# Performance work log

Measured on AMD Instinct MI355X. Metric: run time of the kernel, lower is better.

## Reference

```python
import math
import jax, jax.numpy as jnp
import numpy as np

BATCH, L, H, M, K = 16, 4096, 256, 256, 4

def setup_inputs() -> dict:
    key = jax.random.key(0)
    ks = jax.random.split(key, 12)
    inputs = jax.random.normal(ks[0], (BATCH, L, H), jnp.float32)
    b_std = 1.0 / math.sqrt(H)
    c_std = 1.0 / math.sqrt(M)
    B_param = jax.random.uniform(ks[1], (M, H, 2), jnp.float32, -b_std, b_std)
    C_param = jax.random.uniform(ks[2], (H, M, 2), jnp.float32, -c_std, c_std)
    D = jax.random.normal(ks[3], (H,), jnp.float32)
    enc_w = jax.random.normal(ks[4], (H, H), jnp.float32) * (1.0 / math.sqrt(H))
    enc_b = jnp.zeros((H,), jnp.float32)
    conv_w = jax.random.normal(ks[5], (H, 1, K), jnp.float32) * (1.0 / math.sqrt(K))
    conv_b = jnp.zeros((H,), jnp.float32)
    # ring init: r in [0.9,1.0], theta in (0,pi)
    r0 = jnp.sqrt(jax.random.uniform(ks[6], (M,), jnp.float32) * (1.0 - 0.81) + 0.81)
    r0 = jnp.clip(r0, 0.9, 0.999)
    th0 = jax.random.uniform(ks[7], (M,), jnp.float32, 0.05, math.pi - 0.05)
    r_logit_base = jnp.log(r0 / (1.0 - r0))
    th_atanh_base = jnp.arctanh(th0 / math.pi)
    # heads are zero-init in the module; use small random so the selective path is exercised
    r_head_w = jax.random.normal(ks[8], (M, H), jnp.float32) * 0.01
    th_head_w = jax.random.normal(ks[9], (M, H), jnp.float32) * 0.01
    dt_base = jax.random.normal(ks[10], (M,), jnp.float32) * 0.5
    inj_head_w = jax.random.normal(ks[11], (M, H), jnp.float32) * 0.01
    return {"inputs": inputs, "B_param": B_param, "C_param": C_param, "D": D,
            "enc_w": enc_w, "enc_b": enc_b, "conv_w": conv_w, "conv_b": conv_b,
            "r_logit_base": r_logit_base, "th_atanh_base": th_atanh_base,
            "r_head_w": r_head_w, "th_head_w": th_head_w, "dt_base": dt_base,
            "inj_head_w": inj_head_w}

def _forward(inputs, B_param, C_param, D, enc_w, enc_b, conv_w, conv_b,
             r_logit_base, th_atanh_base, r_head_w, th_head_w, dt_base, inj_head_w):
    silu = jax.nn.silu
    # encoder: linear -> SiLU -> depthwise causal conv (left pad K-1) -> SiLU
    feats = silu(inputs @ enc_w.T + enc_b)                      # (B,L,H)
    fc = jnp.transpose(feats, (0, 2, 1))                        # (B,H,L)
    conv = jax.lax.conv_general_dilated(
        fc, conv_w, window_strides=(1,), padding=[(K - 1, 0)],
        dimension_numbers=("NCH", "OIH", "NCH"), feature_group_count=H)
    feats = silu(jnp.transpose(conv + conv_b[None, :, None], (0, 2, 1)))  # (B,L,H)
    # spectral conditioning
    r = jax.nn.sigmoid(r_logit_base + feats @ r_head_w.T)       # (B,L,M)
    theta = math.pi * jnp.tanh(th_atanh_base + feats @ th_head_w.T)
    dt = jax.nn.sigmoid(dt_base)                                # (M,) per_step_dt=False
    dtc = jnp.maximum(dt, 1e-6)
    r2 = jnp.maximum(r * r, 1e-8)
    A = jnp.maximum((r2 - 2.0 * r * jnp.cos(theta) + 1.0) / (dtc * dtc * r2), 0.0)
    G = jnp.maximum((1.0 - r2) / (dtc * r2), 0.0)
    # complex input projection + selective injection gate
    bu = jax.lax.complex(inputs @ B_param[..., 0].T, inputs @ B_param[..., 1].T)  # (B,L,M) c64
    gate = jax.nn.sigmoid(feats @ inj_head_w.T)
    bu = bu * gate
    # time-major for scan
    A_s = jnp.transpose(A, (1, 0, 2))
    G_s = jnp.transpose(G, (1, 0, 2))
    bu_s = jnp.transpose(bu, (1, 0, 2))
    z0 = jnp.zeros((inputs.shape[0], M), jnp.complex64)
    x0 = jnp.zeros((inputs.shape[0], M), jnp.complex64)

    def step(carry, t_in):  # imex1 variant
        z, x = carry
        A_t, G_t, bu_t = t_in
        S = 1.0 + dtc * G_t
        z = (z + dtc * (-A_t * x + bu_t)) / jnp.maximum(S, 1e-6)
        x = x + dtc * z
        return (z, x), x

    _, xs = jax.lax.scan(step, (z0, x0), (A_s, G_s, bu_s))      # (L,B,M) complex64
    proj = (jnp.einsum("lbm,hm->lbh", xs.real, C_param[..., 0])
            - jnp.einsum("lbm,hm->lbh", xs.imag, C_param[..., 1]))
    proj = jnp.transpose(proj, (1, 0, 2))                       # (B,L,H)
    return proj + D * inputs

def reference(inputs, B_param, C_param, D, enc_w, enc_b, conv_w, conv_b,
              r_logit_base, th_atanh_base, r_head_w, th_head_w, dt_base, inj_head_w):
    return _forward(inputs, B_param, C_param, D, enc_w, enc_b, conv_w, conv_b,
                    r_logit_base, th_atanh_base, r_head_w, th_head_w, dt_base, inj_head_w)
```

## Files before the change

### kernel.cpp

```cpp
#include <hip/hip_runtime.h>

#define H_ 256
#define M_ 256
#define L_ 4096
#define B_ 16
#define PI_F 3.14159265358979323846f

typedef unsigned short u16;
typedef __attribute__((ext_vector_type(8))) short short8v;
typedef __attribute__((ext_vector_type(4))) float floatx4;

__device__ __forceinline__ float sigm(float x) { return 1.0f / (1.0f + expf(-x)); }
__device__ __forceinline__ u16 f2bf(float f) {
    unsigned int u = __float_as_uint(f);
    unsigned int r = (u + 0x7fff + ((u >> 16) & 1)) >> 16;
    return (u16)r;
}
__device__ __forceinline__ float bf2f(u16 h) { return __uint_as_float(((unsigned int)h) << 16); }
__device__ __forceinline__ void split2(float x, u16& h, u16& l) {
    h = f2bf(x);
    l = f2bf(x - bf2f(h));
}

__global__ __launch_bounds__(256) void k_prep(const float* __restrict__ Bp,
                                              const float* __restrict__ Cp,
                                              const float* __restrict__ enc_w,
                                              const float* __restrict__ Wr,
                                              const float* __restrict__ Wt,
                                              const float* __restrict__ Wg,
                                              const float* __restrict__ dtb,
                                              u16* __restrict__ EWhi, u16* __restrict__ EWlo,
                                              u16* __restrict__ HWhi, u16* __restrict__ HWlo,
                                              u16* __restrict__ GWhi,
                                              u16* __restrict__ WBh,
                                              u16* __restrict__ Chath,
                                              float* __restrict__ dtc, float* __restrict__ idt,
                                              float* __restrict__ idt2) {
    int tid = blockIdx.x * 256 + threadIdx.x;
    if (tid < M_) {
        float d = fmaxf(sigm(dtb[tid]), 1e-6f);
        dtc[tid] = d;
        idt[tid] = 1.0f / d;
        idt2[tid] = 1.0f / (d * d);
    }
    u16 h, l;
    split2(enc_w[tid], h, l); EWhi[tid] = h; EWlo[tid] = l;
    split2(Wr[tid], h, l);    HWhi[tid] = h; HWlo[tid] = l;
    split2(Wt[tid], h, l);    HWhi[65536 + tid] = h; HWlo[65536 + tid] = l;
    GWhi[tid] = f2bf(Wg[tid]);
    WBh[tid]         = f2bf(Bp[2 * tid + 0]);
    WBh[65536 + tid] = f2bf(Bp[2 * tid + 1]);
    int hh = tid >> 8, m = tid & (M_ - 1);
    Chath[hh * 512 + 2 * m + 0] = f2bf(Cp[2 * tid + 0]);
    Chath[hh * 512 + 2 * m + 1] = f2bf(-Cp[2 * tid + 1]);
}

__global__ __launch_bounds__(256) void k_zero(float* __restrict__ p, int n) {
    int i = blockIdx.x * 256 + threadIdx.x;
    if (i < n) p[i] = 0.0f;
}

__global__ __launch_bounds__(256) void k_tobf(const float* __restrict__ X, u16* __restrict__ Y) {
    size_t i = ((size_t)blockIdx.x * 256 + threadIdx.x) * 8;
    float4 a = *(const float4*)&X[i];
    float4 b = *(const float4*)&X[i + 4];
    u16 o[8] = {f2bf(a.x), f2bf(a.y), f2bf(a.z), f2bf(a.w),
                f2bf(b.x), f2bf(b.y), f2bf(b.z), f2bf(b.w)};
    *(short8v*)&Y[i] = *(short8v*)o;
}

template <int NH, int NPROD, int EPI, bool AGLOB>
__global__ __launch_bounds__(256) void k_sgemm(const float* __restrict__ A,
                                               const u16* __restrict__ Whi,
                                               const u16* __restrict__ Wlo,
                                               float* __restrict__ OUT,
                                               const float* __restrict__ p0,
                                               const float* __restrict__ p1,
                                               const float* __restrict__ p2,
                                               const float* __restrict__ p3,
                                               int K, int C, int t0) {
    constexpr int LOR = (NPROD == 3) ? 128 : 1;
    __shared__ u16 Ah[128][40];
    __shared__ u16 Al[LOR][40];
    __shared__ u16 Bh[NH][128][40];
    __shared__ u16 Bl[(NPROD == 3) ? NH : 1][128][40];
    const int tid = threadIdx.x;
    const int tpb = C >> 7;
    const int batch = blockIdx.y / tpb;
    const int i0 = (blockIdx.y % tpb) << 7;
    const int colBase = blockIdx.x << 7;
    const int aRow0 = AGLOB ? (batch * L_ + t0 + i0) : (batch * C + i0);
    const int oRow0 = batch * C + i0;
    const int arow = tid >> 1, aseg = (tid & 1) << 4;
    const float* pa = &A[(size_t)(aRow0 + arow) * K + aseg];
    float4 ra0 = *(const float4*)pa, ra1 = *(const float4*)(pa + 4);
    float4 ra2 = *(const float4*)(pa + 8), ra3 = *(const float4*)(pa + 12);
    const int lane = tid & 63, wv = tid >> 6;
    const int wr = wv >> 1, wc = wv & 1;
    const int fr = lane & 15, kg = lane >> 4;
    floatx4 acc[NH][4][4];
#pragma unroll
    for (int h = 0; h < NH; ++h)
#pragma unroll
        for (int i = 0; i < 4; ++i)
#pragma unroll
            for (int j = 0; j < 4; ++j) acc[h][i][j] = (floatx4){0.f, 0.f, 0.f, 0.f};
    const int KT = K >> 5;
    for (int kt = 0; kt < KT; ++kt) {
        short8v rbh[NH][2], rbl[(NPROD == 3) ? NH : 1][2];
#pragma unroll
        for (int h = 0; h < NH; ++h) {
            const u16* pb = &Whi[(size_t)h * 65536 + (size_t)(colBase + arow) * K + kt * 32 + aseg];
            rbh[h][0] = *(const short8v*)pb; rbh[h][1] = *(const short8v*)(pb + 8);
            if (NPROD == 3) {
                const u16* pl = &Wlo[(size_t)h * 65536 + (size_t)(colBase + arow) * K + kt * 32 + aseg];
                rbl[h][0] = *(const short8v*)pl; rbl[h][1] = *(const short8v*)(pl + 8);
            }
        }
        __syncthreads();
        {
            u16 hb[16], lb[16];
            float v[16] = {ra0.x, ra0.y, ra0.z, ra0.w, ra1.x, ra1.y, ra1.z, ra1.w,
                           ra2.x, ra2.y, ra2.z, ra2.w, ra3.x, ra3.y, ra3.z, ra3.w};
#pragma unroll
            for (int s = 0; s < 16; ++s) {
                if (NPROD == 3) split2(v[s], hb[s], lb[s]);
                else hb[s] = f2bf(v[s]);
            }
            *(short8v*)&Ah[arow][aseg] = *(short8v*)&hb[0];
            *(short8v*)&Ah[arow][aseg + 8] = *(short8v*)&hb[8];
            if (NPROD == 3) {
                *(short8v*)&Al[arow][aseg] = *(short8v*)&lb[0];
                *(short8v*)&Al[arow][aseg + 8] = *(short8v*)&lb[8];
            }
        }
#pragma unroll
        for (int h = 0; h < NH; ++h) {
            *(short8v*)&Bh[h][arow][aseg] = rbh[h][0];
            *(short8v*)&Bh[h][arow][aseg + 8] = rbh[h][1];
            if (NPROD == 3) {
                *(short8v*)&Bl[h][arow][aseg] = rbl[h][0];
                *(short8v*)&Bl[h][arow][aseg + 8] = rbl[h][1];
            }
        }
        __syncthreads();
        if (kt + 1 < KT) {
            pa += 32;
            ra0 = *(const float4*)pa; ra1 = *(const float4*)(pa + 4);
            ra2 = *(const float4*)(pa + 8); ra3 = *(const float4*)(pa + 12);
        }
        short8v afh[4], afl[4];
#pragma unroll
        for (int i = 0; i < 4; ++i) afh[i] = *(short8v*)&Ah[wr * 64 + i * 16 + fr][kg << 3];
        if (NPROD == 3) {
#pragma unroll
            for (int i = 0; i < 4; ++i) afl[i] = *(short8v*)&Al[wr * 64 + i * 16 + fr][kg << 3];
        }
#pragma unroll
        for (int h = 0; h < NH; ++h) {
            short8v bfh[4], bfl[4];
#pragma unroll
            for (int j = 0; j < 4; ++j) bfh[j] = *(short8v*)&Bh[h][wc * 64 + j * 16 + fr][kg << 3];
            if (NPROD == 3) {
#pragma unroll
                for (int j = 0; j < 4; ++j) bfl[j] = *(short8v*)&Bl[h][wc * 64 + j * 16 + fr][kg << 3];
            }
#pragma unroll
            for (int i = 0; i < 4; ++i)
#pragma unroll
                for (int j = 0; j < 4; ++j) {
                    floatx4 t = acc[h][i][j];
                    if (NPROD == 3) {
                        t = __builtin_amdgcn_mfma_f32_16x16x32_bf16(afl[i], bfh[j], t, 0, 0, 0);
                        t = __builtin_amdgcn_mfma_f32_16x16x32_bf16(afh[i], bfl[j], t, 0, 0, 0);
                    }
                    t = __builtin_amdgcn_mfma_f32_16x16x32_bf16(afh[i], bfh[j], t, 0, 0, 0);
                    acc[h][i][j] = t;
                }
        }
    }
#pragma unroll
    for (int i = 0; i < 4; ++i)
#pragma unroll
        for (int j = 0; j < 4; ++j) {
            int rbase = wr * 64 + i * 16 + (kg << 2);
            int col = colBase + wc * 64 + j * 16 + fr;
#pragma unroll
            for (int r = 0; r < 4; ++r) {
                int orow = oRow0 + rbase + r;
                if (EPI == 1) {
                    float v = acc[0][i][j][r] + p0[col];
                    OUT[(size_t)orow * 256 + col] = v * sigm(v);
                } else if (EPI == 2) {
                    OUT[(size_t)orow * 256 + col] = sigm(acc[0][i][j][r]);
                } else {
                    float rr = sigm(p0[col] + acc[0][i][j][r]);
                    float th = PI_F * tanhf(p1[col] + acc[1][i][j][r]);
                    float r2 = fmaxf(rr * rr, 1e-8f);
                    float Av = fmaxf((r2 - 2.0f * rr * cosf(th) + 1.0f) * p3[col] / r2, 0.0f);
                    float Gv = fmaxf((1.0f - r2) * p2[col] / r2, 0.0f);
                    *(float2*)&OUT[((size_t)orow * 256 + col) * 2] = make_float2(Av, Gv);
                }
            }
        }
}

template <int EPI>
__global__ __launch_bounds__(256) void k_mgemm(const u16* __restrict__ A,
                                               const u16* __restrict__ W,
                                               float* __restrict__ OUT,
                                               const float* __restrict__ GT,
                                               const float* __restrict__ Dv,
                                               const float* __restrict__ X0,
                                               int K, int N, int C, int t0) {
    __shared__ u16 As[128][40];
    __shared__ u16 Bs[128][40];
    const int tid = threadIdx.x;
    const int tpb = C >> 7;
    const int batch = blockIdx.y / tpb;
    const int i0 = (blockIdx.y % tpb) << 7;
    const int colBase = blockIdx.x << 7;
    const int aRow0 = (EPI == 0) ? (batch * L_ + t0 + i0) : (batch * C + i0);
    const int oRow0 = (EPI == 0) ? (batch * C + i0) : (batch * L_ + t0 + i0);
    const int arow = tid >> 1, aseg = (tid & 1) << 4;
    const u16* pa = &A[(size_t)(aRow0 + arow) * K + aseg];
    const u16* pb = &W[(size_t)(colBase + arow) * K + aseg];
    short8v ra0 = *(const short8v*)pa, ra1 = *(const short8v*)(pa + 8);
    short8v rb0 = *(const short8v*)pb, rb1 = *(const short8v*)(pb + 8);
    const int lane = tid & 63, wv = tid >> 6;
    const int wr = wv >> 1, wc = wv & 1;
    const int fr = lane & 15, kg = lane >> 4;
    floatx4 acc[4][4];
#pragma unroll
    for (int i = 0; i < 4; ++i)
#pragma unroll
        for (int j = 0; j < 4; ++j) acc[i][j] = (floatx4){0.f, 0.f, 0.f, 0.f};
    const int KT = K >> 5;
    for (int kt = 0; kt < KT; ++kt) {
        __syncthreads();
        *(short8v*)&As[arow][aseg] = ra0; *(short8v*)&As[arow][aseg + 8] = ra1;
        *(short8v*)&Bs[arow][aseg] = rb0; *(short8v*)&Bs[arow][aseg + 8] = rb1;
        __syncthreads();
        if (kt + 1 < KT) {
            pa += 32; pb += 32;
            ra0 = *(const short8v*)pa; ra1 = *(const short8v*)(pa + 8);
            rb0 = *(const short8v*)pb; rb1 = *(const short8v*)(pb + 8);
        }
        short8v af[4], bf[4];
#pragma unroll
        for (int i = 0; i < 4; ++i) af[i] = *(short8v*)&As[wr * 64 + i * 16 + fr][kg << 3];
#pragma unroll
        for (int j = 0; j < 4; ++j) bf[j] = *(short8v*)&Bs[wc * 64 + j * 16 + fr][kg << 3];
#pragma unroll
        for (int i = 0; i < 4; ++i)
#pragma unroll
            for (int j = 0; j < 4; ++j)
                acc[i][j] = __builtin_amdgcn_mfma_f32_16x16x32_bf16(af[i], bf[j], acc[i][j], 0, 0, 0);
    }
#pragma unroll
    for (int i = 0; i < 4; ++i)
#pragma unroll
        for (int j = 0; j < 4; ++j) {
            int rbase = wr * 64 + i * 16 + (kg << 2);
            int col = colBase + wc * 64 + j * 16 + fr;
#pragma unroll
            for (int r = 0; r < 4; ++r) {
                int lrow = rbase + r;
                float v = acc[i][j][r];
                if (EPI == 0) {
                    int orow = oRow0 + lrow;
                    float g = GT[(size_t)orow * 256 + (col & 255)];
                    OUT[(size_t)orow * N + col] = v * g;
                } else {
                    int grow = oRow0 + lrow;
                    OUT[(size_t)grow * 256 + col] = fmaf(Dv[col], X0[(size_t)grow * 256 + col], v);
                }
            }
        }
}

__global__ __launch_bounds__(256) void k_conv(const float* __restrict__ F0,
                                              const float* __restrict__ TAIL,
                                              const float* __restrict__ cw,
                                              const float* __restrict__ cb,
                                              float* __restrict__ F,
                                              int t0, int C) {
    int idx = blockIdx.x * 256 + threadIdx.x;
    int h = idx & (H_ - 1);
    int rl = idx >> 8;
    int b = rl / C;
    int dtl = rl - b * C;
    int t = t0 + dtl;
    float w0 = cw[h * 4 + 0], w1 = cw[h * 4 + 1], w2 = cw[h * 4 + 2], w3 = cw[h * 4 + 3];
    float acc = cb[h];
    acc = fmaf(F0[(size_t)rl * H_ + h], w3, acc);
#pragma unroll
    for (int kk = 1; kk <= 3; ++kk) {
        float w = (kk == 1) ? w2 : (kk == 2) ? w1 : w0;
        if (t - kk >= 0) {
            float src;
            if (dtl - kk >= 0) src = F0[(size_t)(rl - kk) * H_ + h];
            else               src = TAIL[((b * 3 + (3 + dtl - kk)) << 8) + h];
            acc = fmaf(src, w, acc);
        }
    }
    F[(size_t)rl * H_ + h] = acc * sigm(acc);
}

__global__ __launch_bounds__(256) void k_tail(const float* __restrict__ F0,
                                              float* __restrict__ TAIL, int C) {
    int b = blockIdx.x / 3, j = blockIdx.x % 3, h = threadIdx.x;
    TAIL[((b * 3 + j) << 8) + h] = F0[((size_t)(b * C + C - 3 + j) << 8) + h];
}

#define SEG_ 64
__global__ __launch_bounds__(256) void k_scan1(const float* __restrict__ AGf2,
                                               const float* __restrict__ BU,
                                               const float* __restrict__ dtc_,
                                               float* __restrict__ SEGM,
                                               float* __restrict__ SEGV,
                                               int C) {
    int m = threadIdx.x;
    int nseg = C >> 6;
    int b = blockIdx.x / nseg;
    int s = blockIdx.x - b * nseg;
    float dt = dtc_[m];
    size_t row0 = (size_t)b * C + s * SEG_;
    float a = 1.f, bb = 0.f, c = 0.f, d = 1.f;
    float vzr = 0.f, vzi = 0.f, vxr = 0.f, vxi = 0.f;
    for (int t = 0; t < SEG_; ++t) {
        size_t row = row0 + t;
        float2 ag = *(const float2*)&AGf2[(row * 256 + m) * 2];
        float br = BU[row * 512 + m];
        float bi = BU[row * 512 + 256 + m];
        float S = fmaf(dt, ag.y, 1.0f);
        float e = 1.0f / fmaxf(S, 1e-6f);
        float sa = e;
        float sb = -dt * ag.x * e;
        float sc = dt * e;
        float sd = fmaf(dt, sb, 1.0f);
        float na = fmaf(sa, a, sb * c), nb = fmaf(sa, bb, sb * d);
        float nc = fmaf(sc, a, sd * c), nd = fmaf(sc, bb, sd * d);
        float wz = dt * e;
        float nvzr = fmaf(sa, vzr, fmaf(sb, vxr, wz * br));
        float nvzi = fmaf(sa, vzi, fmaf(sb, vxi, wz * bi));
        float nvxr = fmaf(sc, vzr, fmaf(sd, vxr, dt * wz * br));
        float nvxi = fmaf(sc, vzi, fmaf(sd, vxi, dt * wz * bi));
        a = na; bb = nb; c = nc; d = nd;
        vzr = nvzr; vzi = nvzi; vxr = nvxr; vxi = nvxi;
    }
    size_t o = ((size_t)blockIdx.x * M_ + m) * 4;
    *(float4*)&SEGM[o] = make_float4(a, bb, c, d);
    *(float4*)&SEGV[o] = make_float4(vzr, vzi, vxr, vxi);
}

__global__ __launch_bounds__(256) void k_scan2(const float* __restrict__ SEGM,
                                               const float* __restrict__ SEGV,
                                               float* __restrict__ carry,
                                               float* __restrict__ PRE,
                                               int C) {
    int m = threadIdx.x;
    int b = blockIdx.x;
    int nseg = C >> 6;
    float4 st = *(float4*)&carry[(size_t)(b * M_ + m) * 4];
    for (int s = 0; s < nseg; ++s) {
        size_t o = ((size_t)(b * nseg + s) * M_ + m) * 4;
        *(float4*)&PRE[o] = st;
        float4 Mm = *(const float4*)&SEGM[o];
        float4 Vv = *(const float4*)&SEGV[o];
        float nzr = fmaf(Mm.x, st.x, fmaf(Mm.y, st.z, Vv.x));
        float nzi = fmaf(Mm.x, st.y, fmaf(Mm.y, st.w, Vv.y));
        float nxr = fmaf(Mm.z, st.x, fmaf(Mm.w, st.z, Vv.z));
        float nxi = fmaf(Mm.z, st.y, fmaf(Mm.w, st.w, Vv.w));
        st = make_float4(nzr, nzi, nxr, nxi);
    }
    *(float4*)&carry[(size_t)(b * M_ + m) * 4] = st;
}

__global__ __launch_bounds__(256) void k_scan3(const float* __restrict__ AGf2,
                                               const float* __restrict__ BU,
                                               const float* __restrict__ dtc_,
                                               const float* __restrict__ PRE,
                                               u16* __restrict__ XSh,
                                               int C) {
    int m = threadIdx.x;
    int nseg = C >> 6;
    int b = blockIdx.x / nseg;
    int s = blockIdx.x - b * nseg;
    float dt = dtc_[m];
    float4 st = *(const float4*)&PRE[((size_t)blockIdx.x * M_ + m) * 4];
    float zr = st.x, zi = st.y, xr = st.z, xi = st.w;
    size_t row0 = (size_t)b * C + s * SEG_;
    for (int t = 0; t < SEG_; ++t) {
        size_t row = row0 + t;
        float2 ag = *(const float2*)&AGf2[(row * 256 + m) * 2];
        float br = BU[row * 512 + m];
        float bi = BU[row * 512 + 256 + m];
        float S = fmaf(dt, ag.y, 1.0f);
        float inv = 1.0f / fmaxf(S, 1e-6f);
        zr = fmaf(dt, fmaf(-ag.x, xr, br), zr) * inv;
        zi = fmaf(dt, fmaf(-ag.x, xi, bi), zi) * inv;
        xr = fmaf(dt, zr, xr);
        xi = fmaf(dt, zi, xi);
        unsigned int pk = (unsigned int)f2bf(xr) | ((unsigned int)f2bf(xi) << 16);
        *(unsigned int*)&XSh[row * 512 + 2 * m] = pk;
    }
}

extern "C" void kernel_launch(void* const* d_in, const int* in_sizes, int n_in,
                              void* d_out, int out_size, void* d_ws, size_t ws_size,
                              hipStream_t stream) {
    const float* inputs = (const float*)d_in[0];
    const float* Bp     = (const float*)d_in[1];
    const float* Cp     = (const float*)d_in[2];
    const float* Dv     = (const float*)d_in[3];
    const float* enc_w  = (const float*)d_in[4];
    const float* enc_b  = (const float*)d_in[5];
    const float* conv_w = (const float*)d_in[6];
    const float* conv_b = (const float*)d_in[7];
    const float* rlb    = (const float*)d_in[8];
    const float* tab    = (const float*)d_in[9];
    const float* Wr     = (const float*)d_in[10];
    const float* Wt     = (const float*)d_in[11];
    const float* dtb    = (const float*)d_in[12];
    const float* Wg     = (const float*)d_in[13];

    int C = 4096;
    while (C > 128) {
        size_t need = (size_t)B_ * C * 8704 + (80ull << 20);
        if (need <= ws_size) break;
        C >>= 1;
    }

    char* ws = (char*)d_ws;
    size_t off = 0;
    auto alloc = [&](size_t bytes) -> char* {
        char* p = ws + off;
        off = (off + bytes + 1023) & ~(size_t)1023;
        return p;
    };
    const int rows = B_ * C;
    const int nseg = C >> 6;
    float* F0   = (float*)alloc((size_t)rows * 256 * 4);
    float* F    = (float*)alloc((size_t)rows * 256 * 4);
    float* AGf2 = (float*)alloc((size_t)rows * 512 * 4);
    float* GT   = (float*)alloc((size_t)rows * 256 * 4);
    float* BU   = (float*)alloc((size_t)rows * 512 * 4);
    u16*   Xbf  = (u16*)alloc((size_t)B_ * L_ * 256 * 2);
    u16*   XSh  = (u16*)alloc((size_t)rows * 512 * 2);
    float* SEGM = (float*)alloc((size_t)B_ * nseg * M_ * 16);
    float* SEGV = (float*)alloc((size_t)B_ * nseg * M_ * 16);
    float* PRE  = (float*)alloc((size_t)B_ * nseg * M_ * 16);
    u16* EWhi = (u16*)alloc(65536 * 2);
    u16* EWlo = (u16*)alloc(65536 * 2);
    u16* HWhi = (u16*)alloc(2 * 65536 * 2);
    u16* HWlo = (u16*)alloc(2 * 65536 * 2);
    u16* GWhi = (u16*)alloc(65536 * 2);
    u16* WBh  = (u16*)alloc(2 * 65536 * 2);
    u16* Chath= (u16*)alloc(2 * 65536 * 2);
    float* dtc  = (float*)alloc(1024);
    float* idt  = (float*)alloc(1024);
    float* idt2 = (float*)alloc(1024);
    float* carry= (float*)alloc(B_ * M_ * 16);
    float* TAIL = (float*)alloc(B_ * 3 * 256 * 4);

    const int NC = L_ / C;
    const int tpb = C >> 7;

    k_prep<<<256, 256, 0, stream>>>(Bp, Cp, enc_w, Wr, Wt, Wg, dtb,
                                    EWhi, EWlo, HWhi, HWlo, GWhi, WBh, Chath, dtc, idt, idt2);
    k_zero<<<(B_ * M_ * 4 + 255) / 256, 256, 0, stream>>>(carry, B_ * M_ * 4);
    k_tobf<<<(B_ * L_ * 256) / (256 * 8), 256, 0, stream>>>(inputs, Xbf);

    for (int c = 0; c < NC; ++c) {
        int t0 = c * C;
        k_sgemm<1, 3, 1, true><<<dim3(2, B_ * tpb), 256, 0, stream>>>(
            inputs, EWhi, EWlo, F0, enc_b, nullptr, nullptr, nullptr, 256, C, t0);
        k_conv<<<rows, 256, 0, stream>>>(F0, TAIL, conv_w, conv_b, F, t0, C);
        k_tail<<<B_ * 3, 256, 0, stream>>>(F0, TAIL, C);
        k_sgemm<2, 3, 0, false><<<dim3(2, B_ * tpb), 256, 0, stream>>>(
            F, HWhi, HWlo, AGf2, rlb, tab, idt, idt2, 256, C, t0);
        k_sgemm<1, 1, 2, false><<<dim3(2, B_ * tpb), 256, 0, stream>>>(
            F, GWhi, nullptr, GT, nullptr, nullptr, nullptr, nullptr, 256, C, t0);
        k_mgemm<0><<<dim3(4, B_ * tpb), 256, 0, stream>>>(
            Xbf, WBh, BU, GT, nullptr, nullptr, 256, 512, C, t0);
        k_scan1<<<B_ * nseg, 256, 0, stream>>>(AGf2, BU, dtc, SEGM, SEGV, C);
        k_scan2<<<B_, 256, 0, stream>>>(SEGM, SEGV, carry, PRE, C);
        k_scan3<<<B_ * nseg, 256, 0, stream>>>(AGf2, BU, dtc, PRE, XSh, C);
        k_mgemm<1><<<dim3(2, B_ * tpb), 256, 0, stream>>>(
            XSh, Chath, (float*)d_out, nullptr, Dv, inputs, 512, 256, C, t0);
    }
}
```

Baseline: 873.6 us.

## Fuse output projection into scan pass and store gate/BU intermediates in bf16

The output projection GEMM is fused into the final scan kernel. Each block now stages 32 timesteps of the bf16 state in shared memory and runs an MFMA against C_param, so the XSh round-trip through global memory and a separate GEMM launch are gone. The bf16 conversion pass over the inputs is dropped because the B-projection now runs through the float-input GEMM template, which converts on the fly. The gate and bu intermediates are stored as bf16 instead of fp32, which cuts memory traffic and workspace and allows larger chunks. The cost is extra bf16 rounding of bu, and a fused kernel with low MFMA parallelism (32 rows per tile) that reloads C from global for every segment.

```diff
diff --git a/kernel.cpp b/kernel.cpp
--- a/kernel.cpp
+++ b/kernel.cpp
@@ -60,30 +60,23 @@
     if (i < n) p[i] = 0.0f;
 }
 
-__global__ __launch_bounds__(256) void k_tobf(const float* __restrict__ X, u16* __restrict__ Y) {
-    size_t i = ((size_t)blockIdx.x * 256 + threadIdx.x) * 8;
-    float4 a = *(const float4*)&X[i];
-    float4 b = *(const float4*)&X[i + 4];
-    u16 o[8] = {f2bf(a.x), f2bf(a.y), f2bf(a.z), f2bf(a.w),
-                f2bf(b.x), f2bf(b.y), f2bf(b.z), f2bf(b.w)};
-    *(short8v*)&Y[i] = *(short8v*)o;
-}
-
 template <int NH, int NPROD, int EPI, bool AGLOB>
 __global__ __launch_bounds__(256) void k_sgemm(const float* __restrict__ A,
                                                const u16* __restrict__ Whi,
                                                const u16* __restrict__ Wlo,
-                                               float* __restrict__ OUT,
+                                               void* __restrict__ OUTv,
+                                               const u16* __restrict__ g16,
                                                const float* __restrict__ p0,
                                                const float* __restrict__ p1,
                                                const float* __restrict__ p2,
                                                const float* __restrict__ p3,
                                                int K, int C, int t0) {
     constexpr int LOR = (NPROD == 3) ? 128 : 1;
+    constexpr int NBL = (NPROD == 3) ? NH : 1;
     __shared__ u16 Ah[128][40];
     __shared__ u16 Al[LOR][40];
     __shared__ u16 Bh[NH][128][40];
-    __shared__ u16 Bl[(NPROD == 3) ? NH : 1][128][40];
+    __shared__ u16 Bl[NBL][LOR][40];
     const int tid = threadIdx.x;
     const int tpb = C >> 7;
     const int batch = blockIdx.y / tpb;
@@ -107,7 +100,7 @@
             for (int j = 0; j < 4; ++j) acc[h][i][j] = (floatx4){0.f, 0.f, 0.f, 0.f};
     const int KT = K >> 5;
     for (int kt = 0; kt < KT; ++kt) {
-        short8v rbh[NH][2], rbl[(NPROD == 3) ? NH : 1][2];
+        short8v rbh[NH][2], rbl[NBL][2];
 #pragma unroll
         for (int h = 0; h < NH; ++h) {
             const u16* pb = &Whi[(size_t)h * 65536 + (size_t)(colBase + arow) * K + kt * 32 + aseg];
@@ -190,90 +183,21 @@
                 int orow = oRow0 + rbase + r;
                 if (EPI == 1) {
                     float v = acc[0][i][j][r] + p0[col];
-                    OUT[(size_t)orow * 256 + col] = v * sigm(v);
+                    ((float*)OUTv)[(size_t)orow * 256 + col] = v * sigm(v);
                 } else if (EPI == 2) {
-                    OUT[(size_t)orow * 256 + col] = sigm(acc[0][i][j][r]);
-                } else {
+                    ((u16*)OUTv)[(size_t)orow * 256 + col] = f2bf(sigm(acc[0][i][j][r]));
+                } else if (EPI == 0) {
                     float rr = sigm(p0[col] + acc[0][i][j][r]);
                     float th = PI_F * tanhf(p1[col] + acc[1][i][j][r]);
                     float r2 = fmaxf(rr * rr, 1e-8f);
                     float Av = fmaxf((r2 - 2.0f * rr * cosf(th) + 1.0f) * p3[col] / r2, 0.0f);
                     float Gv = fmaxf((1.0f - r2) * p2[col] / r2, 0.0f);
-                    *(float2*)&OUT[((size_t)orow * 256 + col) * 2] = make_float2(Av, Gv);
-                }
-            }
-        }
-}
-
-template <int EPI>
-__global__ __launch_bounds__(256) void k_mgemm(const u16* __restrict__ A,
-                                               const u16* __restrict__ W,
-                                               float* __restrict__ OUT,
-                                               const float* __restrict__ GT,
-                                               const float* __restrict__ Dv,
-                                               const float* __restrict__ X0,
-                                               int K, int N, int C, int t0) {
-    __shared__ u16 As[128][40];
-    __shared__ u16 Bs[128][40];
-    const int tid = threadIdx.x;
-    const int tpb = C >> 7;
-    const int batch = blockIdx.y / tpb;
-    const int i0 = (blockIdx.y % tpb) << 7;
-    const int colBase = blockIdx.x << 7;
-    const int aRow0 = (EPI == 0) ? (batch * L_ + t0 + i0) : (batch * C + i0);
-    const int oRow0 = (EPI == 0) ? (batch * C + i0) : (batch * L_ + t0 + i0);
-    const int arow = tid >> 1, aseg = (tid & 1) << 4;
-    const u16* pa = &A[(size_t)(aRow0 + arow) * K + aseg];
-    const u16* pb = &W[(size_t)(colBase + arow) * K + aseg];
-    short8v ra0 = *(const short8v*)pa, ra1 = *(const short8v*)(pa + 8);
-    short8v rb0 = *(const short8v*)pb, rb1 = *(const short8v*)(pb + 8);
-    const int lane = tid & 63, wv = tid >> 6;
-    const int wr = wv >> 1, wc = wv & 1;
-    const int fr = lane & 15, kg = lane >> 4;
-    floatx4 acc[4][4];
-#pragma unroll
-    for (int i = 0; i < 4; ++i)
-#pragma unroll
-        for (int j = 0; j < 4; ++j) acc[i][j] = (floatx4){0.f, 0.f, 0.f, 0.f};
-    const int KT = K >> 5;
-    for (int kt = 0; kt < KT; ++kt) {
-        __syncthreads();
-        *(short8v*)&As[arow][aseg] = ra0; *(short8v*)&As[arow][aseg + 8] = ra1;
-        *(short8v*)&Bs[arow][aseg] = rb0; *(short8v*)&Bs[arow][aseg + 8] = rb1;
-        __syncthreads();
-        if (kt + 1 < KT) {
-            pa += 32; pb += 32;
-            ra0 = *(const short8v*)pa; ra1 = *(const short8v*)(pa + 8);
-            rb0 = *(const short8v*)pb; rb1 = *(const short8v*)(pb + 8);
-        }
-        short8v af[4], bf[4];
-#pragma unroll
-        for (int i = 0; i < 4; ++i) af[i] = *(short8v*)&As[wr * 64 + i * 16 + fr][kg << 3];
-#pragma unroll
-        for (int j = 0; j < 4; ++j) bf[j] = *(short8v*)&Bs[wc * 64 + j * 16 + fr][kg << 3];
-#pragma unroll
-        for (int i = 0; i < 4; ++i)
-#pragma unroll
-            for (int j = 0; j < 4; ++j)
-                acc[i][j] = __builtin_amdgcn_mfma_f32_16x16x32_bf16(af[i], bf[j], acc[i][j], 0, 0, 0);
-    }
-#pragma unroll
-    for (int i = 0; i < 4; ++i)
-#pragma unroll
-        for (int j = 0; j < 4; ++j) {
-            int rbase = wr * 64 + i * 16 + (kg << 2);
-            int col = colBase + wc * 64 + j * 16 + fr;
-#pragma unroll
-            for (int r = 0; r < 4; ++r) {
-                int lrow = rbase + r;
-                float v = acc[i][j][r];
-                if (EPI == 0) {
-                    int orow = oRow0 + lrow;
-                    float g = GT[(size_t)orow * 256 + (col & 255)];
-                    OUT[(size_t)orow * N + col] = v * g;
+                    *(float2*)&((float*)OUTv)[((size_t)orow * 256 + col) * 2] = make_float2(Av, Gv);
                 } else {
-                    int grow = oRow0 + lrow;
-                    OUT[(size_t)grow * 256 + col] = fmaf(Dv[col], X0[(size_t)grow * 256 + col], v);
+                    float g = bf2f(g16[(size_t)orow * 256 + col]);
+#pragma unroll
+                    for (int h = 0; h < NH; ++h)
+                        ((u16*)OUTv)[(size_t)orow * 512 + h * 256 + col] = f2bf(acc[h][i][j][r] * g);
                 }
             }
         }
@@ -315,7 +239,7 @@
 
 #define SEG_ 64
 __global__ __launch_bounds__(256) void k_scan1(const float* __restrict__ AGf2,
-                                               const float* __restrict__ BU,
+                                               const u16* __restrict__ BUh,
                                                const float* __restrict__ dtc_,
                                                float* __restrict__ SEGM,
                                                float* __restrict__ SEGV,
@@ -331,8 +255,8 @@
     for (int t = 0; t < SEG_; ++t) {
         size_t row = row0 + t;
         float2 ag = *(const float2*)&AGf2[(row * 256 + m) * 2];
-        float br = BU[row * 512 + m];
-        float bi = BU[row * 512 + 256 + m];
+        float br = bf2f(BUh[row * 512 + m]);
+        float bi = bf2f(BUh[row * 512 + 256 + m]);
         float S = fmaf(dt, ag.y, 1.0f);
         float e = 1.0f / fmaxf(S, 1e-6f);
         float sa = e;
@@ -377,33 +301,87 @@
     *(float4*)&carry[(size_t)(b * M_ + m) * 4] = st;
 }
 
-__global__ __launch_bounds__(256) void k_scan3(const float* __restrict__ AGf2,
-                                               const float* __restrict__ BU,
-                                               const float* __restrict__ dtc_,
-                                               const float* __restrict__ PRE,
-                                               u16* __restrict__ XSh,
-                                               int C) {
-    int m = threadIdx.x;
-    int nseg = C >> 6;
-    int b = blockIdx.x / nseg;
-    int s = blockIdx.x - b * nseg;
-    float dt = dtc_[m];
+__global__ __launch_bounds__(256) void k_scan3p(const float* __restrict__ AGf2,
+                                                const u16* __restrict__ BUh,
+                                                const float* __restrict__ dtc_,
+                                                const float* __restrict__ PRE,
+                                                const u16* __restrict__ Chath,
+                                                const float* __restrict__ Dv,
+                                                const float* __restrict__ X0,
+                                                float* __restrict__ OUT,
+                                                int t0, int C) {
+    __shared__ u16 XT[32][520];
+    __shared__ u16 Bs[256][40];
+    const int tid = threadIdx.x;
+    const int m = tid;
+    const int nseg = C >> 6;
+    const int b = blockIdx.x / nseg;
+    const int s = blockIdx.x - b * nseg;
+    const float dt = dtc_[m];
     float4 st = *(const float4*)&PRE[((size_t)blockIdx.x * M_ + m) * 4];
     float zr = st.x, zi = st.y, xr = st.z, xi = st.w;
-    size_t row0 = (size_t)b * C + s * SEG_;
-    for (int t = 0; t < SEG_; ++t) {
-        size_t row = row0 + t;
-        float2 ag = *(const float2*)&AGf2[(row * 256 + m) * 2];
-        float br = BU[row * 512 + m];
-        float bi = BU[row * 512 + 256 + m];
-        float S = fmaf(dt, ag.y, 1.0f);
-        float inv = 1.0f / fmaxf(S, 1e-6f);
-        zr = fmaf(dt, fmaf(-ag.x, xr, br), zr) * inv;
-        zi = fmaf(dt, fmaf(-ag.x, xi, bi), zi) * inv;
-        xr = fmaf(dt, zr, xr);
-        xi = fmaf(dt, zi, xi);
-        unsigned int pk = (unsigned int)f2bf(xr) | ((unsigned int)f2bf(xi) << 16);
-        *(unsigned int*)&XSh[row * 512 + 2 * m] = pk;
+    const size_t row0 = (size_t)b * C + s * SEG_;
+    const int grow0 = b * L_ + t0 + s * SEG_;
+    const int lane = tid & 63, wc = tid >> 6;
+    const int fr = lane & 15, kg = lane >> 4;
+#pragma unroll
+    for (int half = 0; half < 2; ++half) {
+        for (int t = 0; t < 32; ++t) {
+            size_t row = row0 + half * 32 + t;
+            float2 ag = *(const float2*)&AGf2[(row * 256 + m) * 2];
+            float br = bf2f(BUh[row * 512 + m]);
+            float bi = bf2f(BUh[row * 512 + 256 + m]);
+            float S = fmaf(dt, ag.y, 1.0f);
+            float inv = 1.0f / fmaxf(S, 1e-6f);
+            zr = fmaf(dt, fmaf(-ag.x, xr, br), zr) * inv;
+            zi = fmaf(dt, fmaf(-ag.x, xi, bi), zi) * inv;
+            xr = fmaf(dt, zr, xr);
+            xi = fmaf(dt, zi, xi);
+            unsigned int pk = (unsigned int)f2bf(xr) | ((unsigned int)f2bf(xi) << 16);
+            *(unsigned int*)&XT[t][2 * m] = pk;
+        }
+        __syncthreads();
+        floatx4 pacc[2][4];
+#pragma unroll
+        for (int i = 0; i < 2; ++i)
+#pragma unroll
+            for (int j = 0; j < 4; ++j) pacc[i][j] = (floatx4){0.f, 0.f, 0.f, 0.f};
+        for (int kc = 0; kc < 16; ++kc) {
+            const u16* pc = &Chath[(size_t)tid * 512 + kc * 32];
+            short8v c0 = *(const short8v*)pc;
+            short8v c1 = *(const short8v*)(pc + 8);
+            short8v c2 = *(const short8v*)(pc + 16);
+            short8v c3 = *(const short8v*)(pc + 24);
+            *(short8v*)&Bs[tid][0]  = c0;
+            *(short8v*)&Bs[tid][8]  = c1;
+            *(short8v*)&Bs[tid][16] = c2;
+            *(short8v*)&Bs[tid][24] = c3;
+            __syncthreads();
+            short8v af[2], bf[4];
+#pragma unroll
+            for (int i = 0; i < 2; ++i) af[i] = *(short8v*)&XT[i * 16 + fr][kc * 32 + (kg << 3)];
+#pragma unroll
+            for (int j = 0; j < 4; ++j) bf[j] = *(short8v*)&Bs[wc * 64 + j * 16 + fr][kg << 3];
+#pragma unroll
+            for (int i = 0; i < 2; ++i)
+#pragma unroll
+                for (int j = 0; j < 4; ++j)
+                    pacc[i][j] = __builtin_amdgcn_mfma_f32_16x16x32_bf16(af[i], bf[j], pacc[i][j], 0, 0, 0);
+            __syncthreads();
+        }
+#pragma unroll
+        for (int i = 0; i < 2; ++i)
+#pragma unroll
+            for (int j = 0; j < 4; ++j) {
+                int col = wc * 64 + j * 16 + fr;
+#pragma unroll
+                for (int r = 0; r < 4; ++r) {
+                    int grow = grow0 + half * 32 + i * 16 + (kg << 2) + r;
+                    OUT[(size_t)grow * 256 + col] =
+                        fmaf(Dv[col], X0[(size_t)grow * 256 + col], pacc[i][j][r]);
+                }
+            }
+        __syncthreads();
     }
 }
 
@@ -427,7 +405,7 @@
 
     int C = 4096;
     while (C > 128) {
-        size_t need = (size_t)B_ * C * 8704 + (80ull << 20);
+        size_t need = (size_t)B_ * C * 5632 + (48ull << 20);
         if (need <= ws_size) break;
         C >>= 1;
     }
@@ -444,10 +422,8 @@
     float* F0   = (float*)alloc((size_t)rows * 256 * 4);
     float* F    = (float*)alloc((size_t)rows * 256 * 4);
     float* AGf2 = (float*)alloc((size_t)rows * 512 * 4);
-    float* GT   = (float*)alloc((size_t)rows * 256 * 4);
-    float* BU   = (float*)alloc((size_t)rows * 512 * 4);
-    u16*   Xbf  = (u16*)alloc((size_t)B_ * L_ * 256 * 2);
-    u16*   XSh  = (u16*)alloc((size_t)rows * 512 * 2);
+    u16*   GTh  = (u16*)alloc((size_t)rows * 256 * 2);
+    u16*   BUh  = (u16*)alloc((size_t)rows * 512 * 2);
     float* SEGM = (float*)alloc((size_t)B_ * nseg * M_ * 16);
     float* SEGV = (float*)alloc((size_t)B_ * nseg * M_ * 16);
     float* PRE  = (float*)alloc((size_t)B_ * nseg * M_ * 16);
@@ -470,24 +446,22 @@
     k_prep<<<256, 256, 0, stream>>>(Bp, Cp, enc_w, Wr, Wt, Wg, dtb,
                                     EWhi, EWlo, HWhi, HWlo, GWhi, WBh, Chath, dtc, idt, idt2);
     k_zero<<<(B_ * M_ * 4 + 255) / 256, 256, 0, stream>>>(carry, B_ * M_ * 4);
-    k_tobf<<<(B_ * L_ * 256) / (256 * 8), 256, 0, stream>>>(inputs, Xbf);
 
     for (int c = 0; c < NC; ++c) {
         int t0 = c * C;
         k_sgemm<1, 3, 1, true><<<dim3(2, B_ * tpb), 256, 0, stream>>>(
-            inputs, EWhi, EWlo, F0, enc_b, nullptr, nullptr, nullptr, 256, C, t0);
+            inputs, EWhi, EWlo, F0, nullptr, enc_b, nullptr, nullptr, nullptr, 256, C, t0);
         k_conv<<<rows, 256, 0, stream>>>(F0, TAIL, conv_w, conv_b, F, t0, C);
         k_tail<<<B_ * 3, 256, 0, stream>>>(F0, TAIL, C);
         k_sgemm<2, 3, 0, false><<<dim3(2, B_ * tpb), 256, 0, stream>>>(
-            F, HWhi, HWlo, AGf2, rlb, tab, idt, idt2, 256, C, t0);
+            F, HWhi, HWlo, AGf2, nullptr, rlb, tab, idt, idt2, 256, C, t0);
         k_sgemm<1, 1, 2, false><<<dim3(2, B_ * tpb), 256, 0, stream>>>(
-            F, GWhi, nullptr, GT, nullptr, nullptr, nullptr, nullptr, 256, C, t0);
-        k_mgemm<0><<<dim3(4, B_ * tpb), 256, 0, stream>>>(
-            Xbf, WBh, BU, GT, nullptr, nullptr, 256, 512, C, t0);
-        k_scan1<<<B_ * nseg, 256, 0, stream>>>(AGf2, BU, dtc, SEGM, SEGV, C);
+            F, GWhi, nullptr, GTh, nullptr, nullptr, nullptr, nullptr, nullptr, 256, C, t0);
+        k_sgemm<2, 1, 3, true><<<dim3(2, B_ * tpb), 256, 0, stream>>>(
+            inputs, WBh, nullptr, BUh, GTh, nullptr, nullptr, nullptr, nullptr, 256, C, t0);
+        k_scan1<<<B_ * nseg, 256, 0, stream>>>(AGf2, BUh, dtc, SEGM, SEGV, C);
         k_scan2<<<B_, 256, 0, stream>>>(SEGM, SEGV, carry, PRE, C);
-        k_scan3<<<B_ * nseg, 256, 0, stream>>>(AGf2, BU, dtc, PRE, XSh, C);
-        k_mgemm<1><<<dim3(2, B_ * tpb), 256, 0, stream>>>(
-            XSh, Chath, (float*)d_out, nullptr, Dv, inputs, 512, 256, C, t0);
-    }
-}
+        k_scan3p<<<B_ * nseg, 256, 0, stream>>>(AGf2, BUh, dtc, PRE, Chath, Dv, inputs,
+                                                (float*)d_out, t0, C);
+    }
+}
```

Result: faster. 725.1 us (-17.0%).
